# Kernel tuning notes

Hardware: AMD Instinct MI355X
Metric: run time of the kernel (lower is better)

The kernel has to match this reference:

```python
import jax, jax.numpy as jnp
import numpy as np

L, B, D = 512, 32, 256  # seq_len, batch (hardcoded 32 in source), in_size == hidden_size
H = D


def setup_inputs() -> dict:
    key = jax.random.key(0)
    ks = jax.random.split(key, 9)
    s_in = 1.0 / np.sqrt(D)
    s_h = 1.0 / np.sqrt(H)
    return {
        "v": jax.random.normal(ks[0], (L, B, D), jnp.float32),
        "h0": jax.random.normal(ks[1], (B, H), jnp.float32),       # torch.randn h
        "Vvec": jax.random.normal(ks[2], (B, H), jnp.float32),     # torch.randn V (squeezed [B,H,1])
        "Wp": jax.random.normal(ks[3], (H, D), jnp.float32) * s_in,   # nn.Linear(D,H,bias=False).weight
        "Wp_": jax.random.normal(ks[4], (H, D), jnp.float32) * s_in,
        "W_ih": jax.random.normal(ks[5], (3 * H, D), jnp.float32) * s_h,  # GRUCell weight_ih
        "W_hh": jax.random.normal(ks[6], (3 * H, H), jnp.float32) * s_h,
        "b_ih": jax.random.normal(ks[7], (3 * H,), jnp.float32) * s_h,
        "b_hh": jax.random.normal(ks[8], (3 * H,), jnp.float32) * s_h,
    }


def _gru_cell(c, h, W_ih, W_hh, b_ih, b_hh):
    # torch.nn.GRUCell math
    gi = c @ W_ih.T + b_ih   # [B, 3H]
    gh = h @ W_hh.T + b_hh   # [B, 3H]
    i_r, i_z, i_n = jnp.split(gi, 3, axis=1)
    h_r, h_z, h_n = jnp.split(gh, 3, axis=1)
    r = jax.nn.sigmoid(i_r + h_r)
    z = jax.nn.sigmoid(i_z + h_z)
    n = jnp.tanh(i_n + r * h_n)
    return (1.0 - z) * n + z * h


def reference(v, h0, Vvec, Wp, Wp_, W_ih, W_hh, b_ih, b_hh):
    # Hoist the two linear projections out of the scan (they don't depend on h).
    xq = jnp.einsum('lbd,hd->lbh', v, Wp)    # Wp(v[i]) for all i
    xv = jnp.einsum('lbd,hd->lbh', v, Wp_)   # Wp_(v), reused every step

    def step(h, xq_i):
        x = jnp.tanh(xq_i[None, :, :] + xv)          # [L, B, H]
        s = jnp.einsum('lbh,bh->bl', x, Vvec)        # attention scores over L
        a = jax.nn.softmax(s, axis=1)                # [B, L]
        c = jnp.einsum('bl,lbd->bd', a, v)           # context [B, D]
        h_new = _gru_cell(c, h, W_ih, W_hh, b_ih, b_hh)
        return h_new, h_new

    _, hs = jax.lax.scan(step, h0, xq)  # hs: [L, B, H]
    # dropout is identity in eval mode
    return hs
```

## Files before the change

### kernel.cpp

```cpp
#include <hip/hip_runtime.h>
#include <stdint.h>


#define C2    2.8853900817779268f
#define LOG2E 1.4426950408889634f

typedef __fp16 f16x2 __attribute__((ext_vector_type(2)));

static __device__ __forceinline__ float rcp_f(float x)  { return __builtin_amdgcn_rcpf(x); }
static __device__ __forceinline__ float exp2_f(float x) { return __builtin_amdgcn_exp2f(x); }
static __device__ __forceinline__ uint32_t pk16(float a, float b) {
  f16x2 p = __builtin_amdgcn_cvt_pkrtz(a, b);
  return __builtin_bit_cast(uint32_t, p);
}
static __device__ __forceinline__ float dot2f(uint32_t a, uint32_t b, float c) {
  return __builtin_amdgcn_fdot2(__builtin_bit_cast(f16x2, a),
                                __builtin_bit_cast(f16x2, b), c, false);
}

__global__ __launch_bounds__(256) void gemm_nt(
    const float* __restrict__ A, const float* __restrict__ W,
    const float* __restrict__ bias, float* __restrict__ out,
    int N, int expmode)
{
  __shared__ __align__(16) float As[32][68];
  __shared__ __align__(16) float Ws[32][68];
  const int t = threadIdx.x;
  const int tx = t & 15, ty = t >> 4;
  const int n0 = blockIdx.x * 64, m0 = blockIdx.y * 64;
  float acc[4][4] = {};

  for (int k0 = 0; k0 < 256; k0 += 32) {
#pragma unroll
    for (int s = 0; s < 2; ++s) {
      int f = t + s * 256;
      int row = f >> 3, kq = f & 7;
      float4 a = *(const float4*)&A[(size_t)(m0 + row) * 256 + k0 + kq * 4];
      float4 w = *(const float4*)&W[(size_t)(n0 + row) * 256 + k0 + kq * 4];
      As[kq * 4 + 0][row] = a.x; As[kq * 4 + 1][row] = a.y;
      As[kq * 4 + 2][row] = a.z; As[kq * 4 + 3][row] = a.w;
      Ws[kq * 4 + 0][row] = w.x; Ws[kq * 4 + 1][row] = w.y;
      Ws[kq * 4 + 2][row] = w.z; Ws[kq * 4 + 3][row] = w.w;
    }
    __syncthreads();
#pragma unroll
    for (int kk = 0; kk < 32; ++kk) {
      float4 a4 = *(const float4*)&As[kk][ty * 4];
      float4 b4 = *(const float4*)&Ws[kk][tx * 4];
      float av[4] = {a4.x, a4.y, a4.z, a4.w};
      float bv[4] = {b4.x, b4.y, b4.z, b4.w};
#pragma unroll
      for (int r = 0; r < 4; ++r)
#pragma unroll
        for (int c = 0; c < 4; ++c)
          acc[r][c] = fmaf(av[r], bv[c], acc[r][c]);
    }
    __syncthreads();
  }

#pragma unroll
  for (int r = 0; r < 4; ++r) {
    float4 o;
    if (expmode) {
      o.x = exp2_f(C2 * acc[r][0]); o.y = exp2_f(C2 * acc[r][1]);
      o.z = exp2_f(C2 * acc[r][2]); o.w = exp2_f(C2 * acc[r][3]);
    } else {
      float4 bb = *(const float4*)&bias[n0 + tx * 4];
      o.x = acc[r][0] + bb.x; o.y = acc[r][1] + bb.y;
      o.z = acc[r][2] + bb.z; o.w = acc[r][3] + bb.w;
    }
    *(float4*)&out[(size_t)(m0 + ty * 4 + r) * N + n0 + tx * 4] = o;
  }
}

__global__ __launch_bounds__(256) void score_k(
    const float* __restrict__ Eq, const float* __restrict__ Ev,
    const float* __restrict__ Vvec, float* __restrict__ S)
{
  __shared__ __align__(16) float Eqs[64][68];
  __shared__ __align__(16) float Evs[32][68];
  __shared__ float Vs[256];
  const int t = threadIdx.x;
  const int tx = t & 15, ty = t >> 4;
  const int l0 = blockIdx.x * 32;
  const int i0 = blockIdx.y * 64;
  const int b  = blockIdx.z;

  Vs[t] = -2.0f * Vvec[b * 256 + t];
  float acc[4][2] = {};

  for (int st = 0; st < 4; ++st) {
    const int h0 = st * 64;
#pragma unroll
    for (int s = 0; s < 4; ++s) {
      int f = t + s * 256;
      int row = f >> 4, cq = f & 15;
      *(float4*)&Eqs[row][cq * 4] =
          *(const float4*)&Eq[((size_t)(i0 + row) * 32 + b) * 256 + h0 + cq * 4];
    }
#pragma unroll
    for (int s = 0; s < 2; ++s) {
      int f = t + s * 256;
      int row = f >> 4, cq = f & 15;
      *(float4*)&Evs[row][cq * 4] =
          *(const float4*)&Ev[((size_t)(l0 + row) * 32 + b) * 256 + h0 + cq * 4];
    }
    __syncthreads();
#pragma unroll 8
    for (int kk = 0; kk < 64; ++kk) {
      float vh  = Vs[h0 + kk];
      float ev0 = Evs[tx][kk];
      float ev1 = Evs[tx + 16][kk];
#pragma unroll
      for (int r = 0; r < 4; ++r) {
        float eq = Eqs[ty * 4 + r][kk];
        acc[r][0] += vh * rcp_f(fmaf(eq, ev0, 1.0f));
        acc[r][1] += vh * rcp_f(fmaf(eq, ev1, 1.0f));
      }
    }
    __syncthreads();
  }

#pragma unroll
  for (int r = 0; r < 4; ++r) {
    float* ps = &S[((size_t)b * 512 + i0 + ty * 4 + r) * 512 + l0];
    ps[tx]      = acc[r][0];
    ps[tx + 16] = acc[r][1];
  }
}

__global__ __launch_bounds__(64) void softmax_k(float* __restrict__ S)
{
  const int t = threadIdx.x;
  float* row = &S[(size_t)blockIdx.x * 512];
  float x[8];
  float m = -1e30f;
#pragma unroll
  for (int u = 0; u < 8; ++u) { x[u] = row[t + u * 64]; m = fmaxf(m, x[u]); }
#pragma unroll
  for (int o = 32; o; o >>= 1) m = fmaxf(m, __shfl_xor(m, o, 64));
  float sum = 0.f;
#pragma unroll
  for (int u = 0; u < 8; ++u) { x[u] = exp2_f(LOG2E * (x[u] - m)); sum += x[u]; }
#pragma unroll
  for (int o = 32; o; o >>= 1) sum += __shfl_xor(sum, o, 64);
  float inv = rcp_f(sum);
#pragma unroll
  for (int u = 0; u < 8; ++u) row[t + u * 64] = x[u] * inv;
}

__global__ __launch_bounds__(256) void ctx_k(
    const float* __restrict__ Aw, const float* __restrict__ v,
    float* __restrict__ C)
{
  __shared__ __align__(16) float As[32][68];
  __shared__ __align__(16) float Vs[32][68];
  const int t = threadIdx.x, tx = t & 15, ty = t >> 4;
  const int d0 = blockIdx.x * 64, i0 = blockIdx.y * 64, b = blockIdx.z;
  float acc[4][4] = {};

  for (int l0 = 0; l0 < 512; l0 += 32) {
#pragma unroll
    for (int s = 0; s < 2; ++s) {
      int f = t + s * 256;
      int row = f >> 3, lq = f & 7;
      float4 a = *(const float4*)&Aw[((size_t)b * 512 + i0 + row) * 512 + l0 + lq * 4];
      As[lq * 4 + 0][row] = a.x; As[lq * 4 + 1][row] = a.y;
      As[lq * 4 + 2][row] = a.z; As[lq * 4 + 3][row] = a.w;
    }
#pragma unroll
    for (int s = 0; s < 2; ++s) {
      int f = t + s * 256;
      int row = f >> 4, dq = f & 15;
      *(float4*)&Vs[row][dq * 4] =
          *(const float4*)&v[((size_t)(l0 + row) * 32 + b) * 256 + d0 + dq * 4];
    }
    __syncthreads();
#pragma unroll
    for (int kk = 0; kk < 32; ++kk) {
      float4 a4 = *(const float4*)&As[kk][ty * 4];
      float4 b4 = *(const float4*)&Vs[kk][tx * 4];
      float av[4] = {a4.x, a4.y, a4.z, a4.w};
      float bv[4] = {b4.x, b4.y, b4.z, b4.w};
#pragma unroll
      for (int r = 0; r < 4; ++r)
#pragma unroll
        for (int c = 0; c < 4; ++c)
          acc[r][c] = fmaf(av[r], bv[c], acc[r][c]);
    }
    __syncthreads();
  }

#pragma unroll
  for (int r = 0; r < 4; ++r) {
    float4 o = {acc[r][0], acc[r][1], acc[r][2], acc[r][3]};
    *(float4*)&C[((size_t)(i0 + ty * 4 + r) * 32 + b) * 256 + d0 + tx * 4] = o;
  }
}

__global__ __launch_bounds__(512, 2) void gru_k(
    const float* __restrict__ Gi, const float* __restrict__ Whh,
    const float* __restrict__ bhh, const float* __restrict__ h0,
    float* __restrict__ out)
{
  __shared__ float part[6][256];
  __shared__ __align__(16) _Float16 hsh[256];
  const int t = threadIdx.x, j = t & 255, half = t >> 8, b = blockIdx.x;

  uint32_t wpk[3][64];
#pragma unroll
  for (int g = 0; g < 3; ++g) {
    const float4* wp = (const float4*)&Whh[(size_t)(j + g * 256) * 256 + half * 128];
#pragma unroll
    for (int c = 0; c < 32; ++c) {
      float4 w = wp[c];
      wpk[g][c * 2]     = pk16(w.x, w.y);
      wpk[g][c * 2 + 1] = pk16(w.z, w.w);
    }
  }

  float h_old = 0.f, br = 0.f, bz = 0.f, bn = 0.f;
  if (t < 256) {
    h_old = h0[b * 256 + j];
    hsh[j] = (_Float16)h_old;
    br = bhh[j]; bz = bhh[256 + j]; bn = bhh[512 + j];
  }
  __syncthreads();

  const uint4* h4 = (const uint4*)hsh;
  for (int i = 0; i < 512; ++i) {
    float gr = 0.f, gz = 0.f, gn = 0.f;
    if (t < 256) {
      const float* gp = &Gi[((size_t)i * 32 + b) * 768 + j];
      gr = gp[0]; gz = gp[256]; gn = gp[512];
    }
    float a0 = 0.f, a1 = 0.f, a2 = 0.f;
#pragma unroll
    for (int c = 0; c < 16; ++c) {
      uint4 hh = h4[half * 16 + c];
      uint32_t hx[4] = {hh.x, hh.y, hh.z, hh.w};
#pragma unroll
      for (int u = 0; u < 4; ++u) {
        a0 = dot2f(wpk[0][c * 4 + u], hx[u], a0);
        a1 = dot2f(wpk[1][c * 4 + u], hx[u], a1);
        a2 = dot2f(wpk[2][c * 4 + u], hx[u], a2);
      }
    }
    part[half * 3 + 0][j] = a0;
    part[half * 3 + 1][j] = a1;
    part[half * 3 + 2][j] = a2;
    __syncthreads();
    if (t < 256) {
      float ghr = part[0][j] + part[3][j] + br;
      float ghz = part[1][j] + part[4][j] + bz;
      float ghn = part[2][j] + part[5][j] + bn;
      float r = rcp_f(1.0f + exp2_f(-LOG2E * (gr + ghr)));
      float z = rcp_f(1.0f + exp2_f(-LOG2E * (gz + ghz)));
      float na = fmaf(r, ghn, gn);
      float n = fmaf(-2.0f, rcp_f(1.0f + exp2_f(C2 * na)), 1.0f);
      float hnew = fmaf(z, h_old - n, n);
      h_old = hnew;
      out[((size_t)i * 32 + b) * 256 + j] = hnew;
      hsh[j] = (_Float16)hnew;
    }
    __syncthreads();
  }
}

extern "C" void kernel_launch(void* const* d_in, const int* in_sizes, int n_in,
                              void* d_out, int out_size, void* d_ws, size_t ws_size,
                              hipStream_t stream)
{
  const float* v   = (const float*)d_in[0];
  const float* h0  = (const float*)d_in[1];
  const float* Vv  = (const float*)d_in[2];
  const float* Wp  = (const float*)d_in[3];
  const float* Wp_ = (const float*)d_in[4];
  const float* Wih = (const float*)d_in[5];
  const float* Whh = (const float*)d_in[6];
  const float* bih = (const float*)d_in[7];
  const float* bhh = (const float*)d_in[8];
  float* out = (float*)d_out;
  float* ws  = (float*)d_ws;

  float* Eq = ws;
  float* Ev = ws + 4194304;
  float* S  = ws + 8388608;
  float* C  = ws;
  float* Gi = ws + 4194304;

  gemm_nt<<<dim3(4, 256), 256, 0, stream>>>(v, Wp,  nullptr, Eq, 256, 1);
  gemm_nt<<<dim3(4, 256), 256, 0, stream>>>(v, Wp_, nullptr, Ev, 256, 1);
  score_k<<<dim3(16, 8, 32), 256, 0, stream>>>(Eq, Ev, Vv, S);
  softmax_k<<<16384, 64, 0, stream>>>(S);
  ctx_k<<<dim3(4, 8, 32), 256, 0, stream>>>(S, v, C);
  gemm_nt<<<dim3(12, 256), 256, 0, stream>>>(C, Wih, bih, Gi, 768, 0);
  gru_k<<<32, 512, 0, stream>>>(Gi, Whh, bhh, h0, out);
}
```

Measured before the change: 1.102 ms.

## Split GRU recurrence across 1024 threads, prefetch gate inputs, vectorize score LDS reads

The GRU kernel now runs 1024 threads per batch row. Each thread holds a quarter of the W_hh row in packed fp16, which halves both register use and the serial dot-product length per step. The next step's Gi values are prefetched a step ahead, and h is double-buffered in shared memory. The score kernel reads Eq, Ev and V from LDS as float4 instead of scalars to cut LDS instruction count. The cost is a four-way partial-sum reduction and larger blocks that synchronize every step.

```diff
diff --git a/kernel.cpp b/kernel.cpp
--- a/kernel.cpp
+++ b/kernel.cpp
@@ -79,7 +79,7 @@
 {
   __shared__ __align__(16) float Eqs[64][68];
   __shared__ __align__(16) float Evs[32][68];
-  __shared__ float Vs[256];
+  __shared__ __align__(16) float Vs[256];
   const int t = threadIdx.x;
   const int tx = t & 15, ty = t >> 4;
   const int l0 = blockIdx.x * 32;
@@ -106,16 +106,22 @@
           *(const float4*)&Ev[((size_t)(l0 + row) * 32 + b) * 256 + h0 + cq * 4];
     }
     __syncthreads();
-#pragma unroll 8
-    for (int kk = 0; kk < 64; ++kk) {
-      float vh  = Vs[h0 + kk];
-      float ev0 = Evs[tx][kk];
-      float ev1 = Evs[tx + 16][kk];
+#pragma unroll 4
+    for (int k4 = 0; k4 < 16; ++k4) {
+      float4 vh = *(const float4*)&Vs[h0 + k4 * 4];
+      float4 e0 = *(const float4*)&Evs[tx][k4 * 4];
+      float4 e1 = *(const float4*)&Evs[tx + 16][k4 * 4];
 #pragma unroll
       for (int r = 0; r < 4; ++r) {
-        float eq = Eqs[ty * 4 + r][kk];
-        acc[r][0] += vh * rcp_f(fmaf(eq, ev0, 1.0f));
-        acc[r][1] += vh * rcp_f(fmaf(eq, ev1, 1.0f));
+        float4 eq = *(const float4*)&Eqs[ty * 4 + r][k4 * 4];
+        acc[r][0] += vh.x * rcp_f(fmaf(eq.x, e0.x, 1.0f));
+        acc[r][0] += vh.y * rcp_f(fmaf(eq.y, e0.y, 1.0f));
+        acc[r][0] += vh.z * rcp_f(fmaf(eq.z, e0.z, 1.0f));
+        acc[r][0] += vh.w * rcp_f(fmaf(eq.w, e0.w, 1.0f));
+        acc[r][1] += vh.x * rcp_f(fmaf(eq.x, e1.x, 1.0f));
+        acc[r][1] += vh.y * rcp_f(fmaf(eq.y, e1.y, 1.0f));
+        acc[r][1] += vh.z * rcp_f(fmaf(eq.z, e1.z, 1.0f));
+        acc[r][1] += vh.w * rcp_f(fmaf(eq.w, e1.w, 1.0f));
       }
     }
     __syncthreads();
@@ -198,21 +204,21 @@
   }
 }
 
-__global__ __launch_bounds__(512, 2) void gru_k(
+__global__ __launch_bounds__(1024) void gru_k(
     const float* __restrict__ Gi, const float* __restrict__ Whh,
     const float* __restrict__ bhh, const float* __restrict__ h0,
     float* __restrict__ out)
 {
-  __shared__ float part[6][256];
-  __shared__ __align__(16) _Float16 hsh[256];
-  const int t = threadIdx.x, j = t & 255, half = t >> 8, b = blockIdx.x;
-
-  uint32_t wpk[3][64];
+  __shared__ float part[12][256];
+  __shared__ __align__(16) _Float16 hbuf[2][256];
+  const int t = threadIdx.x, j = t & 255, q = t >> 8, b = blockIdx.x;
+
+  uint32_t wpk[3][32];
 #pragma unroll
   for (int g = 0; g < 3; ++g) {
-    const float4* wp = (const float4*)&Whh[(size_t)(j + g * 256) * 256 + half * 128];
-#pragma unroll
-    for (int c = 0; c < 32; ++c) {
+    const float4* wp = (const float4*)&Whh[(size_t)(j + g * 256) * 256 + q * 64];
+#pragma unroll
+    for (int c = 0; c < 16; ++c) {
       float4 w = wp[c];
       wpk[g][c * 2]     = pk16(w.x, w.y);
       wpk[g][c * 2 + 1] = pk16(w.z, w.w);
@@ -220,24 +226,30 @@
   }
 
   float h_old = 0.f, br = 0.f, bz = 0.f, bn = 0.f;
+  float gr = 0.f, gz = 0.f, gn = 0.f;
   if (t < 256) {
     h_old = h0[b * 256 + j];
-    hsh[j] = (_Float16)h_old;
+    hbuf[0][j] = (_Float16)h_old;
     br = bhh[j]; bz = bhh[256 + j]; bn = bhh[512 + j];
+    const float* gp = &Gi[(size_t)b * 768 + j];
+    gr = gp[0]; gz = gp[256]; gn = gp[512];
   }
   __syncthreads();
 
-  const uint4* h4 = (const uint4*)hsh;
   for (int i = 0; i < 512; ++i) {
-    float gr = 0.f, gz = 0.f, gn = 0.f;
-    if (t < 256) {
-      const float* gp = &Gi[((size_t)i * 32 + b) * 768 + j];
-      gr = gp[0]; gz = gp[256]; gn = gp[512];
-    }
+    float ngr = 0.f, ngz = 0.f, ngn = 0.f;
+    {
+      int ip = (i + 1 < 512) ? (i + 1) : 511;
+      if (t < 256) {
+        const float* gp = &Gi[((size_t)ip * 32 + b) * 768 + j];
+        ngr = gp[0]; ngz = gp[256]; ngn = gp[512];
+      }
+    }
+    const uint4* h4 = (const uint4*)hbuf[i & 1] + q * 8;
     float a0 = 0.f, a1 = 0.f, a2 = 0.f;
 #pragma unroll
-    for (int c = 0; c < 16; ++c) {
-      uint4 hh = h4[half * 16 + c];
+    for (int c = 0; c < 8; ++c) {
+      uint4 hh = h4[c];
       uint32_t hx[4] = {hh.x, hh.y, hh.z, hh.w};
 #pragma unroll
       for (int u = 0; u < 4; ++u) {
@@ -246,14 +258,14 @@
         a2 = dot2f(wpk[2][c * 4 + u], hx[u], a2);
       }
     }
-    part[half * 3 + 0][j] = a0;
-    part[half * 3 + 1][j] = a1;
-    part[half * 3 + 2][j] = a2;
+    part[q * 3 + 0][j] = a0;
+    part[q * 3 + 1][j] = a1;
+    part[q * 3 + 2][j] = a2;
     __syncthreads();
     if (t < 256) {
-      float ghr = part[0][j] + part[3][j] + br;
-      float ghz = part[1][j] + part[4][j] + bz;
-      float ghn = part[2][j] + part[5][j] + bn;
+      float ghr = part[0][j] + part[3][j] + part[6][j] + part[9][j]  + br;
+      float ghz = part[1][j] + part[4][j] + part[7][j] + part[10][j] + bz;
+      float ghn = part[2][j] + part[5][j] + part[8][j] + part[11][j] + bn;
       float r = rcp_f(1.0f + exp2_f(-LOG2E * (gr + ghr)));
       float z = rcp_f(1.0f + exp2_f(-LOG2E * (gz + ghz)));
       float na = fmaf(r, ghn, gn);
@@ -261,8 +273,9 @@
       float hnew = fmaf(z, h_old - n, n);
       h_old = hnew;
       out[((size_t)i * 32 + b) * 256 + j] = hnew;
-      hsh[j] = (_Float16)hnew;
-    }
+      hbuf[(i + 1) & 1][j] = (_Float16)hnew;
+    }
+    gr = ngr; gz = ngz; gn = ngn;
     __syncthreads();
   }
 }
@@ -295,5 +308,5 @@
   softmax_k<<<16384, 64, 0, stream>>>(S);
   ctx_k<<<dim3(4, 8, 32), 256, 0, stream>>>(S, v, C);
   gemm_nt<<<dim3(12, 256), 256, 0, stream>>>(C, Wih, bih, Gi, 768, 0);
-  gru_k<<<32, 512, 0, stream>>>(Gi, Whh, bhh, h0, out);
-}
+  gru_k<<<32, 1024, 0, stream>>>(Gi, Whh, bhh, h0, out);
+}
```

New measurement: 1.149 ms. 4.3% more time.
